# Kernel tuning notes

Measured on AMD Instinct MI355X. Metric: run time of the kernel, lower is better.

Reference implementation:

```python
import jax, jax.numpy as jnp
import numpy as np

# Module hyperparameters (from init_kwargs)
LEARNING_RATE = 0.01  # not used inside compute_weight_update
TAU_PLUS = 20.0
TAU_MINUS = 20.0
A_PLUS = 0.005
A_MINUS = 0.00525
TARGET_RATE = 0.1
HOMEOSTATIC_RATE = 0.001
TAU_HOMEOSTATIC = 1000.0

B, T, N_PRE, N_POST = 16, 8192, 128, 128


def setup_inputs() -> dict:
    key = jax.random.key(0)
    k1, k2, k3 = jax.random.split(key, 3)
    # Bernoulli spike trains at ~target_rate firing probability
    pre_spikes = (jax.random.uniform(k1, (B, T, N_PRE)) < TARGET_RATE).astype(jnp.float32)
    post_spikes = (jax.random.uniform(k2, (B, T, N_POST)) < TARGET_RATE).astype(jnp.float32)
    weights = jax.random.uniform(k3, (N_PRE, N_POST), dtype=jnp.float32)
    return {"pre_spikes": pre_spikes, "post_spikes": post_spikes, "weights": weights, "dt": 1}


def _temporal_corr(x, kernel, pad):
    """Correlate x [B,T,N] along time with 1-D kernel [L], padding pad=(lo,hi)."""
    b, t, n = x.shape
    xr = jnp.moveaxis(x, 1, 2).reshape(b * n, 1, t)  # [B*N, 1, T]
    k = kernel.reshape(1, 1, -1).astype(x.dtype)
    y = jax.lax.conv_general_dilated(
        xr, k, window_strides=(1,), padding=[pad],
        dimension_numbers=("NCH", "OIH", "NCH"))
    return jnp.moveaxis(y.reshape(b, n, t), 2, 1)  # [B,T,N]


def reference(pre_spikes, post_spikes, weights, dt):
    b, t, n_pre = pre_spikes.shape
    dt = float(dt)

    # Homeostatic rate tracking (first call: avg rates initialized to target_rate)
    alpha = dt / TAU_HOMEOSTATIC
    current_post_rate = post_spikes.mean(axis=(0, 1))
    avg_post_rate = (1.0 - alpha) * TARGET_RATE + alpha * current_post_rate

    # Truncated exponential STDP window: tau in 1..min(int(3*tau)-1, ...) = 1..59
    L = int(TAU_PLUS * 3)  # 60 taps (tau=0 tap zeroed)
    taus = jnp.arange(L, dtype=jnp.float32)
    w_plus = jnp.where(taus > 0, A_PLUS * jnp.exp(-taus * dt / TAU_PLUS), 0.0)
    w_minus = jnp.where(taus > 0, A_MINUS * jnp.exp(-taus * dt / TAU_MINUS), 0.0)

    # LTP: post_filt[t] = sum_{tau>=1} w_plus[tau] * post[t+tau] (future, zero-padded)
    post_filt = _temporal_corr(post_spikes, w_plus, (0, L - 1))
    # LTD: pre_filt[t] = sum_{tau>=1} w_minus[tau] * pre[t-tau] (past, zero-padded)
    pre_filt = _temporal_corr(pre_spikes, w_minus[::-1], (L - 1, 0))

    # sum_t mean_b outer(pre[t], post_filt[t]) - outer(pre_filt[t], post[t]), then /T
    ltp = jnp.einsum("btp,btq->pq", pre_spikes, post_filt)
    ltd = jnp.einsum("btp,btq->pq", pre_filt, post_spikes)
    stdp_update = (ltp - ltd) / (b * t)

    # Homeostatic regulation pulls post rate toward target
    post_rate_error = avg_post_rate - TARGET_RATE
    homeostatic_update = -HOMEOSTATIC_RATE * post_rate_error[None, :] * weights

    return stdp_update + homeostatic_update
```

## Files before the change

kernel.cpp:

```cpp
#include <hip/hip_runtime.h>

#define BB 16
#define TT 8192
#define NN 128
constexpr int CHUNK = 128;
constexpr int NCHB  = BB * TT / CHUNK;
constexpr int NBLK  = NCHB / 2;
constexpr int OUTN  = NN * NN;
constexpr int GS    = 132;
constexpr int SLOTS = OUTN / 2;
constexpr int PROWS = 186;
constexpr int NWAVE = 8;
constexpr int WIN   = CHUNK / NWAVE;

typedef _Float16 f16x8 __attribute__((ext_vector_type(8)));
typedef _Float16 f16x2 __attribute__((ext_vector_type(2)));
typedef float    f32x4 __attribute__((ext_vector_type(4)));

__device__ __forceinline__ unsigned short h16(float x) {
    _Float16 h = (_Float16)x;
    return __builtin_bit_cast(unsigned short, h);
}
__device__ __forceinline__ unsigned int pack2(float x, float y) {
    return (unsigned int)h16(x) | ((unsigned int)h16(y) << 16);
}
__device__ __forceinline__ float2 ldL(const unsigned short* p_lds, int m, int q0) {
    const unsigned int v = *(const unsigned int*)&p_lds[m * NN + q0];
    const f16x2 h = __builtin_bit_cast(f16x2, v);
    return make_float2((float)h[0], (float)h[1]);
}

template<bool ATOMIC>
__global__ __launch_bounds__(512, 2)
void stdp_main(const float* __restrict__ pre, const float* __restrict__ post,
               const int* __restrict__ dtp,
               unsigned int* __restrict__ part, float* __restrict__ wpost,
               float* __restrict__ outat)
{
    __shared__ __align__(16) unsigned short bufP[PROWS * NN];
    __shared__ __align__(16) unsigned short bufG[NN * GS];

    const int tid    = threadIdx.x;
    const int bi     = blockIdx.x;
    const int c0g    = bi * 2;
    const int b      = c0g >> 6;
    const int chunk0 = c0g & 63;
    const int t00    = chunk0 * CHUNK;
    const int t01    = t00 + CHUNK;
    const int wv     = tid >> 6;
    const int lane   = tid & 63;

    const float dtf = (float)(*dtp);
    const float r   = expf(-dtf * (1.0f / 20.0f));

    const float* pb = post + (size_t)b * TT * NN;
    const float* ab = pre  + (size_t)b * TT * NN;

    const int sc = tid & 31;
    const int mr = tid >> 5;

    for (int m = mr; m < PROWS; m += 16) {
        const int t = t00 + 1 + m;
        const float4 v = *(const float4*)(pb + (size_t)t * NN + sc * 4);
        *(uint2*)&bufP[m * NN + sc * 4] = make_uint2(pack2(v.x, v.y), pack2(v.z, v.w));
    }
    __syncthreads();

    const int q0   = lane * 2;
    const int base = wv * WIN;

    unsigned int pk0[8], pk1[8];
    float ps0 = 0.f, ps1 = 0.f;
    #define FILTER_PHASE(SRC) {                                               \
        const float r2 = r * r, r3 = r2 * r, r4 = r2 * r2;                    \
        float2 p = ldL(SRC, base + 15, q0);                        \
        ps0 += p.x; ps1 += p.y;                                               \
        float gx0 = r  * p.x, gy0 = r  * p.y;                                 \
        p = ldL(SRC, base + 16, q0);                               \
        float gx1 = r2 * p.x, gy1 = r2 * p.y;                                 \
        p = ldL(SRC, base + 17, q0);                               \
        float gx2 = r3 * p.x, gy2 = r3 * p.y;                                 \
        p = ldL(SRC, base + 18, q0);                               \
        float gx3 = r4 * p.x, gy3 = r4 * p.y;                                 \
        float wA = r * r4, wB = r2 * r4, wC = r3 * r4, wD = r4 * r4;          \
        _Pragma("unroll")                                                     \
        for (int j = 1; j < 15; ++j) {                                        \
            p = ldL(SRC, base + 15 + 4 * j, q0);                              \
            gx0 = fmaf(wA, p.x, gx0); gy0 = fmaf(wA, p.y, gy0);               \
            p = ldL(SRC, base + 16 + 4 * j, q0);                              \
            gx1 = fmaf(wB, p.x, gx1); gy1 = fmaf(wB, p.y, gy1);               \
            p = ldL(SRC, base + 17 + 4 * j, q0);                              \
            gx2 = fmaf(wC, p.x, gx2); gy2 = fmaf(wC, p.y, gy2);               \
            if (j < 14) {                                                     \
                p = ldL(SRC, base + 18 + 4 * j, q0);                          \
                gx3 = fmaf(wD, p.x, gx3); gy3 = fmaf(wD, p.y, gy3);           \
            }                                                                 \
            wA *= r4; wB *= r4; wC *= r4; wD *= r4;                           \
        }                                                                     \
        const float r8 = r4 * r4, r16 = r8 * r8, r32 = r16 * r16;             \
        const float r60 = ((r32 * r16) * r8) * r4;                            \
        float gx = (gx0 + gx1) + (gx2 + gx3);                                 \
        float gy = (gy0 + gy1) + (gy2 + gy3);                                 \
        pk0[7] = (unsigned int)h16(gx) << 16;                                 \
        pk1[7] = (unsigned int)h16(gy) << 16;                                 \
        _Pragma("unroll")                                                     \
        for (int c = 14; c >= 0; --c) {                                       \
            const float2 p1  = ldL(SRC, base + c,      q0);                   \
            const float2 p60 = ldL(SRC, base + c + 59, q0);                   \
            gx = r * (gx + p1.x) - r60 * p60.x;                               \
            gy = r * (gy + p1.y) - r60 * p60.y;                               \
            ps0 += p1.x; ps1 += p1.y;                                         \
            if (c & 1) {                                                      \
                pk0[c >> 1] = (unsigned int)h16(gx) << 16;                    \
                pk1[c >> 1] = (unsigned int)h16(gy) << 16;                    \
            } else {                                                          \
                pk0[c >> 1] |= h16(gx);                                       \
                pk1[c >> 1] |= h16(gy);                                       \
            }                                                                 \
        }                                                                     \
    }
    #define DUMP_G() {                                                        \
        unsigned short* d0 = &bufG[q0 * GS + base];                           \
        unsigned short* d1 = &bufG[(q0 + 1) * GS + base];                     \
        *(uint4*)(d0)      = make_uint4(pk0[0], pk0[1], pk0[2], pk0[3]);      \
        *(uint4*)(d0 + 8)  = make_uint4(pk0[4], pk0[5], pk0[6], pk0[7]);      \
        *(uint2*)(d1)      = make_uint2(pk1[0], pk1[1]);                      \
        *(uint2*)(d1 + 4)  = make_uint2(pk1[2], pk1[3]);                      \
        *(uint2*)(d1 + 8)  = make_uint2(pk1[4], pk1[5]);                      \
        *(uint2*)(d1 + 12) = make_uint2(pk1[6], pk1[7]);                      \
    }

    FILTER_PHASE(bufP)
    DUMP_G()
    __syncthreads();

    const bool tguard = (chunk0 == 62);
    float4 va[12];
    #pragma unroll
    for (int i = 0; i < 12; ++i) {
        const int m = mr + i * 16;
        const int t = t01 + 1 + m;
        va[i] = make_float4(0.f, 0.f, 0.f, 0.f);
        if (m < PROWS && (!tguard || t < TT))
            va[i] = *(const float4*)(pb + (size_t)t * NN + sc * 4);
    }

    const int pr0 = wv * 16;
    f32x4 acc[8];
    #pragma unroll
    for (int qt = 0; qt < 8; ++qt) acc[qt] = (f32x4){0.f, 0.f, 0.f, 0.f};

    #define MFMA_PHASE(T0) {                                                  \
        const float* abase = ab + (size_t)((T0) + (lane >> 4) * 8) * NN + pr0 + (lane & 15); \
        float an[8];                                                          \
        _Pragma("unroll")                                                     \
        for (int j = 0; j < 8; ++j) an[j] = abase[(size_t)j * NN];            \
        _Pragma("unroll")                                                     \
        for (int ks = 0; ks < 4; ++ks) {                                      \
            f16x8 af;                                                         \
            _Pragma("unroll")                                                 \
            for (int j = 0; j < 8; ++j) af[j] = (_Float16)an[j];              \
            if (ks < 3) {                                                     \
                const float* src = abase + (size_t)((ks + 1) * 32) * NN;      \
                _Pragma("unroll")                                             \
                for (int j = 0; j < 8; ++j) an[j] = src[(size_t)j * NN];      \
            }                                                                 \
            const int koff = ks * 32 + (lane >> 4) * 8;                       \
            _Pragma("unroll")                                                 \
            for (int qt = 0; qt < 8; ++qt) {                                  \
                const unsigned short* gp = &bufG[(qt * 16 + (lane & 15)) * GS + koff]; \
                const uint2 lo = *(const uint2*)(gp);                         \
                const uint2 hi = *(const uint2*)(gp + 4);                     \
                const uint4 u  = make_uint4(lo.x, lo.y, hi.x, hi.y);          \
                const f16x8 bf = __builtin_bit_cast(f16x8, u);                \
                acc[qt] = __builtin_amdgcn_mfma_f32_16x16x32_f16(af, bf, acc[qt], 0, 0, 0); \
            }                                                                 \
        }                                                                     \
    }

    MFMA_PHASE(t00)

    #pragma unroll
    for (int i = 0; i < 12; ++i) {
        const int m = mr + i * 16;
        if (m < PROWS)
            *(uint2*)&bufP[m * NN + sc * 4] =
                make_uint2(pack2(va[i].x, va[i].y), pack2(va[i].z, va[i].w));
    }
    __syncthreads();

    FILTER_PHASE(bufP)
    DUMP_G()
    __syncthreads();

    {
        float* psb = (float*)bufP;
        psb[wv * NN + q0]     = ps0;
        psb[wv * NN + q0 + 1] = ps1;
    }

    MFMA_PHASE(t01)
    __syncthreads();

    if (tid < NN) {
        const float* psb = (const float*)bufP;
        float s = 0.f;
        #pragma unroll
        for (int w = 0; w < NWAVE; ++w) s += psb[w * NN + tid];
        if (chunk0 == 0) s += pb[tid];
        if constexpr (ATOMIC) atomicAdd(&wpost[tid], s);
        else wpost[(size_t)bi * NN + tid] = s;
    }

    if constexpr (!ATOMIC) {
        unsigned int* dst = part + ((size_t)bi * 8 + wv) * 1024 + lane;
        #pragma unroll
        for (int qt = 0; qt < 8; ++qt) {
            dst[qt * 128]      = pack2(acc[qt][0], acc[qt][1]);
            dst[qt * 128 + 64] = pack2(acc[qt][2], acc[qt][3]);
        }
    } else {
        #pragma unroll
        for (int qt = 0; qt < 8; ++qt)
            #pragma unroll
            for (int rg = 0; rg < 4; ++rg) {
                const int prow = pr0 + (lane >> 4) * 4 + rg;
                const int qcol = qt * 16 + (lane & 15);
                atomicAdd(&outat[prow * NN + qcol], acc[qt][rg]);
            }
    }
    #undef FILTER_PHASE
    #undef DUMP_G
    #undef MFMA_PHASE
}

__global__ __launch_bounds__(512)
void finalize_ws(const unsigned int* __restrict__ part, const float* __restrict__ wpost,
                 const int* __restrict__ dtp, const float* __restrict__ W,
                 float* __restrict__ out)
{
    __shared__ float2 red[512];
    __shared__ float  hfs[16];
    const int s    = threadIdx.x & 63;
    const int kq   = threadIdx.x >> 6;
    const int slot = blockIdx.x * 64 + s;
    const int qt   = (slot >> 7) & 7;
    const int qbase = qt * 16;

    {
        const int qi = threadIdx.x >> 5;
        const int pr = threadIdx.x & 31;
        float hsum = 0.f;
        const int q = qbase + qi;
        #pragma unroll 4
        for (int k = pr; k < NBLK; k += 32) hsum += wpost[(size_t)k * NN + q];
        #pragma unroll
        for (int off = 16; off; off >>= 1) hsum += __shfl_down(hsum, off, 32);
        if (pr == 0) {
            const float dtf   = (float)(*dtp);
            const float alpha = dtf * 1e-3f;
            hfs[qi] = -0.001f * (alpha * (hsum * (1.0f / (float)(BB * TT)) - 0.1f));
        }
    }

    float sx = 0.f, sy = 0.f;
    #pragma unroll 8
    for (int k = kq * (NBLK / 8); k < (kq + 1) * (NBLK / 8); ++k) {
        const unsigned int v = part[(size_t)k * SLOTS + slot];
        const f16x2 h = __builtin_bit_cast(f16x2, v);
        sx += (float)h[0];
        sy += (float)h[1];
    }
    red[threadIdx.x] = make_float2(sx, sy);
    __syncthreads();
    if (threadIdx.x < 64) {
        float tx = red[s].x, ty = red[s].y;
        #pragma unroll
        for (int g = 1; g < 8; ++g) {
            const float2 v = red[g * 64 + s];
            tx += v.x; ty += v.y;
        }
        const int lane = slot & 63;
        const int rp   = (slot >> 6) & 1;
        const int wv   = slot >> 10;
        const int p    = wv * 16 + ((lane >> 4) << 2) + rp * 2;
        const int qi   = lane & 15;
        const int q    = qbase + qi;
        const float scale = (float)((0.005 - 0.00525) / (double)(BB * TT));
        const float hf = hfs[qi];
        out[p * NN + q]       = fmaf(tx, scale, hf * W[p * NN + q]);
        out[(p + 1) * NN + q] = fmaf(ty, scale, hf * W[(p + 1) * NN + q]);
    }
}

__global__ void finalize_at(const float* __restrict__ wpost, const int* __restrict__ dtp,
                            const float* __restrict__ W, float* __restrict__ out)
{
    const int i = (blockIdx.x * 256 + threadIdx.x) * 2;
    const int q = i & 127;
    const float scale = (float)((0.005 - 0.00525) / (double)(BB * TT));
    const float dtf   = (float)(*dtp);
    const float alpha = dtf * 1e-3f;
    const float inv   = 1.0f / (float)(BB * TT);
    const float hf0   = -0.001f * (alpha * (wpost[q]     * inv - 0.1f));
    const float hf1   = -0.001f * (alpha * (wpost[q + 1] * inv - 0.1f));
    float2 sv = *(const float2*)(out + i);
    float2 w  = *(const float2*)(W + i);
    float2 o;
    o.x = fmaf(sv.x, scale, hf0 * w.x);
    o.y = fmaf(sv.y, scale, hf1 * w.y);
    *(float2*)(out + i) = o;
}

extern "C" void kernel_launch(void* const* d_in, const int* in_sizes, int n_in,
                              void* d_out, int out_size, void* d_ws, size_t ws_size,
                              hipStream_t stream)
{
    const float* pre  = (const float*)d_in[0];
    const float* post = (const float*)d_in[1];
    const float* W    = (const float*)d_in[2];
    const int*   dtp  = (const int*)d_in[3];
    float* out = (float*)d_out;

    const size_t part_bytes  = (size_t)NBLK * SLOTS * sizeof(unsigned int);
    const size_t wpost_bytes = (size_t)NBLK * NN * sizeof(float);
    const size_t need = part_bytes + wpost_bytes;

    if (ws_size >= need) {
        unsigned int* part = (unsigned int*)d_ws;
        float* wpost       = (float*)((char*)d_ws + part_bytes);
        hipLaunchKernelGGL((stdp_main<false>), dim3(NBLK), dim3(512), 0, stream,
                           pre, post, dtp, part, wpost, (float*)nullptr);
        hipLaunchKernelGGL(finalize_ws, dim3(SLOTS / 64), dim3(512), 0, stream,
                           part, wpost, dtp, W, out);
    } else {
        float* wpost = (float*)d_ws;
        hipMemsetAsync(d_out, 0, OUTN * sizeof(float), stream);
        hipMemsetAsync(wpost, 0, NN * sizeof(float), stream);
        hipLaunchKernelGGL((stdp_main<true>), dim3(NBLK), dim3(512), 0, stream,
                           pre, post, dtp, (unsigned int*)nullptr, wpost, out);
        hipLaunchKernelGGL(finalize_at, dim3(OUTN / 512), dim3(256), 0, stream,
                           wpost, dtp, W, out);
    }
}
```

Baseline: 173.4 us.

## Process one 256-step chunk per block, reading post spikes directly from global

Each block now handles a single 256-timestep chunk instead of two 128-step chunks. The LDS staging buffer for post spikes is gone, and the filter phase reads float2 values straight from global memory, with a guarded path near the end of the sequence. Each wave filters 32 timesteps and the MFMA loop runs 8 k-steps over a wider G buffer. This drops the staging pass and extra barriers, but every wave re-reads the overlapping 59-step filter window from global/L2 instead of LDS. It also gives up the overlap of the next chunk's prefetch with the current MFMA phase.

```diff
diff --git a/kernel.cpp b/kernel.cpp
--- a/kernel.cpp
+++ b/kernel.cpp
@@ -3,13 +3,11 @@
 #define BB 16
 #define TT 8192
 #define NN 128
-constexpr int CHUNK = 128;
-constexpr int NCHB  = BB * TT / CHUNK;
-constexpr int NBLK  = NCHB / 2;
+constexpr int CHUNK = 256;
+constexpr int NBLK  = BB * TT / CHUNK;
 constexpr int OUTN  = NN * NN;
-constexpr int GS    = 132;
+constexpr int GS    = 260;
 constexpr int SLOTS = OUTN / 2;
-constexpr int PROWS = 186;
 constexpr int NWAVE = 8;
 constexpr int WIN   = CHUNK / NWAVE;
 
@@ -23,11 +21,6 @@
 }
 __device__ __forceinline__ unsigned int pack2(float x, float y) {
     return (unsigned int)h16(x) | ((unsigned int)h16(y) << 16);
-}
-__device__ __forceinline__ float2 ldL(const unsigned short* p_lds, int m, int q0) {
-    const unsigned int v = *(const unsigned int*)&p_lds[m * NN + q0];
-    const f16x2 h = __builtin_bit_cast(f16x2, v);
-    return make_float2((float)h[0], (float)h[1]);
 }
 
 template<bool ATOMIC>
@@ -37,18 +30,16 @@
                unsigned int* __restrict__ part, float* __restrict__ wpost,
                float* __restrict__ outat)
 {
-    __shared__ __align__(16) unsigned short bufP[PROWS * NN];
     __shared__ __align__(16) unsigned short bufG[NN * GS];
-
-    const int tid    = threadIdx.x;
-    const int bi     = blockIdx.x;
-    const int c0g    = bi * 2;
-    const int b      = c0g >> 6;
-    const int chunk0 = c0g & 63;
-    const int t00    = chunk0 * CHUNK;
-    const int t01    = t00 + CHUNK;
-    const int wv     = tid >> 6;
-    const int lane   = tid & 63;
+    __shared__ float lds_ps[NWAVE * NN];
+
+    const int tid  = threadIdx.x;
+    const int bi   = blockIdx.x;
+    const int b    = bi >> 5;
+    const int ch   = bi & 31;
+    const int t00  = ch * CHUNK;
+    const int wv   = tid >> 6;
+    const int lane = tid & 63;
 
     const float dtf = (float)(*dtp);
     const float r   = expf(-dtf * (1.0f / 20.0f));
@@ -56,43 +47,37 @@
     const float* pb = post + (size_t)b * TT * NN;
     const float* ab = pre  + (size_t)b * TT * NN;
 
-    const int sc = tid & 31;
-    const int mr = tid >> 5;
-
-    for (int m = mr; m < PROWS; m += 16) {
-        const int t = t00 + 1 + m;
-        const float4 v = *(const float4*)(pb + (size_t)t * NN + sc * 4);
-        *(uint2*)&bufP[m * NN + sc * 4] = make_uint2(pack2(v.x, v.y), pack2(v.z, v.w));
-    }
-    __syncthreads();
-
     const int q0   = lane * 2;
     const int base = wv * WIN;
-
-    unsigned int pk0[8], pk1[8];
+    const float* prow = pb + (size_t)(t00 + 1) * NN + q0;
+    const int mlim = TT - 2 - t00;
+
+    unsigned int pk0[16], pk1[16];
     float ps0 = 0.f, ps1 = 0.f;
-    #define FILTER_PHASE(SRC) {                                               \
+    #define LDF(m) (*(const float2*)(prow + (size_t)(m) * NN))
+    #define LDG(m) (((m) <= mlim) ? LDF(m) : make_float2(0.f, 0.f))
+    #define FILTER_BODY(LD) {                                                 \
         const float r2 = r * r, r3 = r2 * r, r4 = r2 * r2;                    \
-        float2 p = ldL(SRC, base + 15, q0);                        \
+        float2 p = LD(base + 31);                                  \
         ps0 += p.x; ps1 += p.y;                                               \
         float gx0 = r  * p.x, gy0 = r  * p.y;                                 \
-        p = ldL(SRC, base + 16, q0);                               \
+        p = LD(base + 32);                                         \
         float gx1 = r2 * p.x, gy1 = r2 * p.y;                                 \
-        p = ldL(SRC, base + 17, q0);                               \
+        p = LD(base + 33);                                         \
         float gx2 = r3 * p.x, gy2 = r3 * p.y;                                 \
-        p = ldL(SRC, base + 18, q0);                               \
+        p = LD(base + 34);                                         \
         float gx3 = r4 * p.x, gy3 = r4 * p.y;                                 \
         float wA = r * r4, wB = r2 * r4, wC = r3 * r4, wD = r4 * r4;          \
         _Pragma("unroll")                                                     \
         for (int j = 1; j < 15; ++j) {                                        \
-            p = ldL(SRC, base + 15 + 4 * j, q0);                              \
+            p = LD(base + 31 + 4 * j);                                        \
             gx0 = fmaf(wA, p.x, gx0); gy0 = fmaf(wA, p.y, gy0);               \
-            p = ldL(SRC, base + 16 + 4 * j, q0);                              \
+            p = LD(base + 32 + 4 * j);                                        \
             gx1 = fmaf(wB, p.x, gx1); gy1 = fmaf(wB, p.y, gy1);               \
-            p = ldL(SRC, base + 17 + 4 * j, q0);                              \
+            p = LD(base + 33 + 4 * j);                                        \
             gx2 = fmaf(wC, p.x, gx2); gy2 = fmaf(wC, p.y, gy2);               \
             if (j < 14) {                                                     \
-                p = ldL(SRC, base + 18 + 4 * j, q0);                          \
+                p = LD(base + 34 + 4 * j);                                    \
                 gx3 = fmaf(wD, p.x, gx3); gy3 = fmaf(wD, p.y, gy3);           \
             }                                                                 \
             wA *= r4; wB *= r4; wC *= r4; wD *= r4;                           \
@@ -101,12 +86,12 @@
         const float r60 = ((r32 * r16) * r8) * r4;                            \
         float gx = (gx0 + gx1) + (gx2 + gx3);                                 \
         float gy = (gy0 + gy1) + (gy2 + gy3);                                 \
-        pk0[7] = (unsigned int)h16(gx) << 16;                                 \
-        pk1[7] = (unsigned int)h16(gy) << 16;                                 \
+        pk0[15] = (unsigned int)h16(gx) << 16;                                \
+        pk1[15] = (unsigned int)h16(gy) << 16;                                \
         _Pragma("unroll")                                                     \
-        for (int c = 14; c >= 0; --c) {                                       \
-            const float2 p1  = ldL(SRC, base + c,      q0);                   \
-            const float2 p60 = ldL(SRC, base + c + 59, q0);                   \
+        for (int c = 30; c >= 0; --c) {                                       \
+            const float2 p1  = LD(base + c);                                  \
+            const float2 p60 = LD(base + c + 59);                             \
             gx = r * (gx + p1.x) - r60 * p60.x;                               \
             gy = r * (gy + p1.y) - r60 * p60.y;                               \
             ps0 += p1.x; ps1 += p1.y;                                         \
@@ -119,30 +104,40 @@
             }                                                                 \
         }                                                                     \
     }
-    #define DUMP_G() {                                                        \
-        unsigned short* d0 = &bufG[q0 * GS + base];                           \
-        unsigned short* d1 = &bufG[(q0 + 1) * GS + base];                     \
-        *(uint4*)(d0)      = make_uint4(pk0[0], pk0[1], pk0[2], pk0[3]);      \
-        *(uint4*)(d0 + 8)  = make_uint4(pk0[4], pk0[5], pk0[6], pk0[7]);      \
-        *(uint2*)(d1)      = make_uint2(pk1[0], pk1[1]);                      \
-        *(uint2*)(d1 + 4)  = make_uint2(pk1[2], pk1[3]);                      \
-        *(uint2*)(d1 + 8)  = make_uint2(pk1[4], pk1[5]);                      \
-        *(uint2*)(d1 + 12) = make_uint2(pk1[6], pk1[7]);                      \
-    }
-
-    FILTER_PHASE(bufP)
-    DUMP_G()
+
+    if (base + 89 <= mlim) {
+        FILTER_BODY(LDF)
+    } else {
+        FILTER_BODY(LDG)
+    }
+
+    {
+        unsigned short* d0 = &bufG[q0 * GS + base];
+        unsigned short* d1 = &bufG[(q0 + 1) * GS + base];
+        *(uint4*)(d0)      = make_uint4(pk0[0],  pk0[1],  pk0[2],  pk0[3]);
+        *(uint4*)(d0 + 8)  = make_uint4(pk0[4],  pk0[5],  pk0[6],  pk0[7]);
+        *(uint4*)(d0 + 16) = make_uint4(pk0[8],  pk0[9],  pk0[10], pk0[11]);
+        *(uint4*)(d0 + 24) = make_uint4(pk0[12], pk0[13], pk0[14], pk0[15]);
+        *(uint2*)(d1)      = make_uint2(pk1[0],  pk1[1]);
+        *(uint2*)(d1 + 4)  = make_uint2(pk1[2],  pk1[3]);
+        *(uint2*)(d1 + 8)  = make_uint2(pk1[4],  pk1[5]);
+        *(uint2*)(d1 + 12) = make_uint2(pk1[6],  pk1[7]);
+        *(uint2*)(d1 + 16) = make_uint2(pk1[8],  pk1[9]);
+        *(uint2*)(d1 + 20) = make_uint2(pk1[10], pk1[11]);
+        *(uint2*)(d1 + 24) = make_uint2(pk1[12], pk1[13]);
+        *(uint2*)(d1 + 28) = make_uint2(pk1[14], pk1[15]);
+        lds_ps[wv * NN + q0]     = ps0;
+        lds_ps[wv * NN + q0 + 1] = ps1;
+    }
     __syncthreads();
 
-    const bool tguard = (chunk0 == 62);
-    float4 va[12];
-    #pragma unroll
-    for (int i = 0; i < 12; ++i) {
-        const int m = mr + i * 16;
-        const int t = t01 + 1 + m;
-        va[i] = make_float4(0.f, 0.f, 0.f, 0.f);
-        if (m < PROWS && (!tguard || t < TT))
-            va[i] = *(const float4*)(pb + (size_t)t * NN + sc * 4);
+    if (tid < NN) {
+        float s = 0.f;
+        #pragma unroll
+        for (int w = 0; w < NWAVE; ++w) s += lds_ps[w * NN + tid];
+        if (ch == 0) s += pb[tid];
+        if constexpr (ATOMIC) atomicAdd(&wpost[tid], s);
+        else wpost[(size_t)bi * NN + tid] = s;
     }
 
     const int pr0 = wv * 16;
@@ -150,66 +145,32 @@
     #pragma unroll
     for (int qt = 0; qt < 8; ++qt) acc[qt] = (f32x4){0.f, 0.f, 0.f, 0.f};
 
-    #define MFMA_PHASE(T0) {                                                  \
-        const float* abase = ab + (size_t)((T0) + (lane >> 4) * 8) * NN + pr0 + (lane & 15); \
-        float an[8];                                                          \
-        _Pragma("unroll")                                                     \
-        for (int j = 0; j < 8; ++j) an[j] = abase[(size_t)j * NN];            \
-        _Pragma("unroll")                                                     \
-        for (int ks = 0; ks < 4; ++ks) {                                      \
-            f16x8 af;                                                         \
-            _Pragma("unroll")                                                 \
-            for (int j = 0; j < 8; ++j) af[j] = (_Float16)an[j];              \
-            if (ks < 3) {                                                     \
-                const float* src = abase + (size_t)((ks + 1) * 32) * NN;      \
-                _Pragma("unroll")                                             \
-                for (int j = 0; j < 8; ++j) an[j] = src[(size_t)j * NN];      \
-            }                                                                 \
-            const int koff = ks * 32 + (lane >> 4) * 8;                       \
-            _Pragma("unroll")                                                 \
-            for (int qt = 0; qt < 8; ++qt) {                                  \
-                const unsigned short* gp = &bufG[(qt * 16 + (lane & 15)) * GS + koff]; \
-                const uint2 lo = *(const uint2*)(gp);                         \
-                const uint2 hi = *(const uint2*)(gp + 4);                     \
-                const uint4 u  = make_uint4(lo.x, lo.y, hi.x, hi.y);          \
-                const f16x8 bf = __builtin_bit_cast(f16x8, u);                \
-                acc[qt] = __builtin_amdgcn_mfma_f32_16x16x32_f16(af, bf, acc[qt], 0, 0, 0); \
-            }                                                                 \
-        }                                                                     \
-    }
-
-    MFMA_PHASE(t00)
-
-    #pragma unroll
-    for (int i = 0; i < 12; ++i) {
-        const int m = mr + i * 16;
-        if (m < PROWS)
-            *(uint2*)&bufP[m * NN + sc * 4] =
-                make_uint2(pack2(va[i].x, va[i].y), pack2(va[i].z, va[i].w));
-    }
-    __syncthreads();
-
-    FILTER_PHASE(bufP)
-    DUMP_G()
-    __syncthreads();
-
     {
-        float* psb = (float*)bufP;
-        psb[wv * NN + q0]     = ps0;
-        psb[wv * NN + q0 + 1] = ps1;
-    }
-
-    MFMA_PHASE(t01)
-    __syncthreads();
-
-    if (tid < NN) {
-        const float* psb = (const float*)bufP;
-        float s = 0.f;
-        #pragma unroll
-        for (int w = 0; w < NWAVE; ++w) s += psb[w * NN + tid];
-        if (chunk0 == 0) s += pb[tid];
-        if constexpr (ATOMIC) atomicAdd(&wpost[tid], s);
-        else wpost[(size_t)bi * NN + tid] = s;
+        const float* abase = ab + (size_t)(t00 + (lane >> 4) * 8) * NN + pr0 + (lane & 15);
+        float an[8];
+        #pragma unroll
+        for (int j = 0; j < 8; ++j) an[j] = abase[(size_t)j * NN];
+        #pragma unroll
+        for (int ks = 0; ks < 8; ++ks) {
+            f16x8 af;
+            #pragma unroll
+            for (int j = 0; j < 8; ++j) af[j] = (_Float16)an[j];
+            if (ks < 7) {
+                const float* src = abase + (size_t)((ks + 1) * 32) * NN;
+                #pragma unroll
+                for (int j = 0; j < 8; ++j) an[j] = src[(size_t)j * NN];
+            }
+            const int koff = ks * 32 + (lane >> 4) * 8;
+            #pragma unroll
+            for (int qt = 0; qt < 8; ++qt) {
+                const unsigned short* gp = &bufG[(qt * 16 + (lane & 15)) * GS + koff];
+                const uint2 lo = *(const uint2*)(gp);
+                const uint2 hi = *(const uint2*)(gp + 4);
+                const uint4 u  = make_uint4(lo.x, lo.y, hi.x, hi.y);
+                const f16x8 bf = __builtin_bit_cast(f16x8, u);
+                acc[qt] = __builtin_amdgcn_mfma_f32_16x16x32_f16(af, bf, acc[qt], 0, 0, 0);
+            }
+        }
     }
 
     if constexpr (!ATOMIC) {
@@ -224,14 +185,14 @@
         for (int qt = 0; qt < 8; ++qt)
             #pragma unroll
             for (int rg = 0; rg < 4; ++rg) {
-                const int prow = pr0 + (lane >> 4) * 4 + rg;
-                const int qcol = qt * 16 + (lane & 15);
-                atomicAdd(&outat[prow * NN + qcol], acc[qt][rg]);
+                const int prow_o = pr0 + (lane >> 4) * 4 + rg;
+                const int qcol   = qt * 16 + (lane & 15);
+                atomicAdd(&outat[prow_o * NN + qcol], acc[qt][rg]);
             }
     }
-    #undef FILTER_PHASE
-    #undef DUMP_G
-    #undef MFMA_PHASE
+    #undef FILTER_BODY
+    #undef LDF
+    #undef LDG
 }
 
 __global__ __launch_bounds__(512)
```

Result: no change. 173.3 us (-0.0%).
